# Kernel tuning notes

Measured on AMD Instinct MI355X. Metric: run time of the kernel, lower is better.

Reference implementation:

```python
import jax, jax.numpy as jnp
import numpy as np

DIM = 1024
HEADS = 16
DIM_HEAD = 64
INNER = HEADS * DIM_HEAD  # 1024
SCALE = DIM_HEAD ** -0.5


def setup_inputs() -> dict:
    key = jax.random.key(0)
    k1, k2, k3, k4 = jax.random.split(key, 4)
    B, N = 4, 2048
    x = jax.random.normal(k1, (B, N, DIM), dtype=jnp.float32)
    # Linear weights stored as [in, out] so y = x @ W (+ b)
    W_qkv = jax.random.normal(k2, (DIM, 3 * INNER), dtype=jnp.float32) * (DIM ** -0.5)
    W_out = jax.random.normal(k3, (INNER, DIM), dtype=jnp.float32) * (INNER ** -0.5)
    b_out = jax.random.normal(k4, (DIM,), dtype=jnp.float32) * 0.01
    return {"x": x, "W_qkv": W_qkv, "W_out": W_out, "b_out": b_out}


def reference(x, W_qkv, W_out, b_out):
    B, N, _ = x.shape
    qkv = x @ W_qkv  # [B, N, 3*INNER]
    q, k, v = jnp.split(qkv, 3, axis=-1)
    # [B, N, H, Dh] -> [B, H, N, Dh]
    reshape = lambda t: t.reshape(B, N, HEADS, DIM_HEAD).transpose(0, 2, 1, 3)
    q, k, v = reshape(q), reshape(k), reshape(v)
    dots = jnp.einsum("bhqd,bhkd->bhqk", q, k) * SCALE  # [B,H,N,N]
    attn = jax.nn.softmax(dots, axis=-1)
    out = jnp.einsum("bhqk,bhkd->bhqd", attn, v)  # [B,H,N,Dh]
    out = out.transpose(0, 2, 1, 3).reshape(B, N, INNER)
    return out @ W_out + b_out
```

## Files before the change

kernel.cpp:

```cpp
#include <hip/hip_runtime.h>


typedef _Float16 half8 __attribute__((ext_vector_type(8)));
typedef __fp16 fp16v2 __attribute__((ext_vector_type(2)));
typedef float floatx4 __attribute__((ext_vector_type(4)));
typedef unsigned short u16;

struct __align__(8) U16x4 { u16 x, y, z, w; };

__device__ __forceinline__ u16 f2h(float f) {
  union { _Float16 h; u16 u; } cv;
  cv.h = (_Float16)f;
  return cv.u;
}

__device__ __forceinline__ void g2l16(const void* g, void* l) {
  __builtin_amdgcn_global_load_lds(
      (const __attribute__((address_space(1))) void*)g,
      (__attribute__((address_space(3))) void*)l, 16, 0, 0);
}

__device__ __forceinline__ int swz(int c) { return (c & 3) ^ ((c >> 3) & 3); }
__device__ __forceinline__ int swz8(int s) { return (s & 7) ^ ((s >> 3) & 7); }

__global__ __launch_bounds__(256) void cast_f32_f16(const float* __restrict__ in,
                                                    u16* __restrict__ out) {
  long long base = ((long long)blockIdx.x * 256 + threadIdx.x) * 8;
  float4 a = *(const float4*)(in + base);
  float4 b = *(const float4*)(in + base + 4);
  U16x4 u0 = {f2h(a.x), f2h(a.y), f2h(a.z), f2h(a.w)};
  U16x4 u1 = {f2h(b.x), f2h(b.y), f2h(b.z), f2h(b.w)};
  *(U16x4*)(out + base) = u0;
  *(U16x4*)(out + base + 4) = u1;
}

__global__ __launch_bounds__(256) void transpose_cast(const float* __restrict__ in,
                                                      u16* __restrict__ out,
                                                      int K, int N) {
  __shared__ u16 ls[64][72];
  const int nTK = K >> 6;
  const int tk = blockIdx.x % nTK;
  const int tn = blockIdx.x / nTK;
  const int tid = threadIdx.x;
#pragma unroll
  for (int i = 0; i < 4; ++i) {
    int idx = i * 256 + tid;
    int r = idx >> 4, c4 = (idx & 15) * 4;
    float4 v = *(const float4*)(in + (long long)(tk * 64 + r) * N + tn * 64 + c4);
    ls[r][c4 + 0] = f2h(v.x);
    ls[r][c4 + 1] = f2h(v.y);
    ls[r][c4 + 2] = f2h(v.z);
    ls[r][c4 + 3] = f2h(v.w);
  }
  __syncthreads();
#pragma unroll
  for (int i = 0; i < 4; ++i) {
    int idx = i * 256 + tid;
    int nr = idx >> 4, kc4 = (idx & 15) * 4;
    U16x4 u = {ls[kc4 + 0][nr], ls[kc4 + 1][nr], ls[kc4 + 2][nr], ls[kc4 + 3][nr]};
    *(U16x4*)(out + (long long)(tn * 64 + nr) * K + tk * 64 + kc4) = u;
  }
}

template <int EPI>
__global__ __launch_bounds__(256, 4) void gemm_f16(const u16* __restrict__ A,
                                                   const u16* __restrict__ Bt,
                                                   u16* __restrict__ O0,
                                                   u16* __restrict__ O1,
                                                   u16* __restrict__ O2,
                                                   float* __restrict__ Of,
                                                   const float* __restrict__ bias) {
  __shared__ __attribute__((aligned(16))) u16 lsA[128 * 64];
  __shared__ __attribute__((aligned(16))) u16 lsB[128 * 64];
  const int tid = threadIdx.x;
  const int lane = tid & 63, wave = tid >> 6;
  const int l15 = lane & 15, quad = lane >> 4;
  const int w7 = l15 & 7;
  const int offk0 = ((quad) ^ w7) * 8;
  const int offk1 = ((4 + quad) ^ w7) * 8;
  const int wm = (wave >> 1) * 64, wn = (wave & 1) * 64;
  const int bm = blockIdx.x & 63;
  const int bn = blockIdx.x >> 6;

  const u16* ga[4];
  const u16* gb[4];
#pragma unroll
  for (int i = 0; i < 4; ++i) {
    int s = i * 256 + tid;
    ga[i] = A + (long long)(bm * 128 + (s >> 3)) * 1024 + swz8(s) * 8;
    gb[i] = Bt + (long long)(bn * 128 + (s >> 3)) * 1024 + swz8(s) * 8;
  }

  floatx4 acc[4][4] = {};

  for (int kt = 0; kt < 16; ++kt) {
    const int ko = kt * 64;
#pragma unroll
    for (int i = 0; i < 4; ++i)
      g2l16(ga[i] + ko, lsA + (i * 256 + wave * 64) * 8);
#pragma unroll
    for (int i = 0; i < 4; ++i)
      g2l16(gb[i] + ko, lsB + (i * 256 + wave * 64) * 8);
    __syncthreads();
#pragma unroll
    for (int ks = 0; ks < 2; ++ks) {
      const int off = ks ? offk1 : offk0;
      half8 af[4], bf[4];
#pragma unroll
      for (int mt = 0; mt < 4; ++mt)
        af[mt] = *(const half8*)(lsA + (wm + mt * 16 + l15) * 64 + off);
#pragma unroll
      for (int nt = 0; nt < 4; ++nt)
        bf[nt] = *(const half8*)(lsB + (wn + nt * 16 + l15) * 64 + off);
#pragma unroll
      for (int mt = 0; mt < 4; ++mt)
#pragma unroll
        for (int nt = 0; nt < 4; ++nt)
          acc[mt][nt] = __builtin_amdgcn_mfma_f32_16x16x32_f16(af[mt], bf[nt], acc[mt][nt], 0, 0, 0);
    }
    __syncthreads();
  }

  if (EPI == 0) {
    const float slq = 0.125f * 1.44269504088896f;
#pragma unroll
    for (int mt = 0; mt < 4; ++mt) {
      int gm = bm * 128 + wm + mt * 16 + quad * 4;
      int b = gm >> 11, n0 = gm & 2047;
#pragma unroll
      for (int nt = 0; nt < 4; ++nt) {
        int gc = bn * 128 + wn + nt * 16 + l15;
        int t = gc >> 10, hd = gc & 1023, h = hd >> 6, d = hd & 63;
        long long bh = (long long)(b * 16 + h);
        if (t == 2) {
          U16x4 u = {f2h(acc[mt][nt][0]), f2h(acc[mt][nt][1]),
                     f2h(acc[mt][nt][2]), f2h(acc[mt][nt][3])};
          *(U16x4*)(O2 + (bh * 64 + d) * 2048 + n0) = u;
        } else {
          float s = (t == 0) ? slq : 1.0f;
          u16* dst = (t == 0 ? O0 : O1) + (bh * 2048 + n0) * 64 + d;
#pragma unroll
          for (int r = 0; r < 4; ++r) dst[r * 64] = f2h(acc[mt][nt][r] * s);
        }
      }
    }
  } else {
#pragma unroll
    for (int mt = 0; mt < 4; ++mt) {
      int gm = bm * 128 + wm + mt * 16 + quad * 4;
#pragma unroll
      for (int nt = 0; nt < 4; ++nt) {
        int gc = bn * 128 + wn + nt * 16 + l15;
        float bv = bias[gc];
#pragma unroll
        for (int r = 0; r < 4; ++r)
          Of[(long long)(gm + r) * 1024 + gc] = acc[mt][nt][r] + bv;
      }
    }
  }
}

__global__ __launch_bounds__(256, 2) void attn_flash(const u16* __restrict__ Qh,
                                                     const u16* __restrict__ Kh,
                                                     const u16* __restrict__ Vt,
                                                     u16* __restrict__ Oh) {
  __shared__ __attribute__((aligned(16))) u16 lsK[2 * 2 * 64 * 32];
  __shared__ __attribute__((aligned(16))) u16 lsV[2 * 2 * 64 * 32];
  __shared__ __attribute__((aligned(16))) u16 lsP[4 * 64 * 32];
  const int tid = threadIdx.x;
  const int lane = tid & 63, wave = tid >> 6;
  const int l15 = lane & 15, quad = lane >> 4;
  const int sw = (l15 >> 1) & 3;
  const int qsw8 = (quad ^ sw) * 8;
  const int bh = blockIdx.x & 63, qt = blockIdx.x >> 6;
  const u16* Qb = Qh + ((long long)bh * 2048 + qt * 256) * 64;
  const u16* Kb = Kh + (long long)bh * 2048 * 64;
  const u16* Vb = Vt + (long long)bh * 64 * 2048;
  u16* lsPw = lsP + wave * 2048;

  half8 qb[4][2];
#pragma unroll
  for (int pass = 0; pass < 2; ++pass) {
#pragma unroll
    for (int i = 0; i < 4; ++i) {
      int c = i * 256 + tid;
      g2l16(Qb + (pass * 128 + ((c >> 2) & 127)) * 64 + (c >> 9) * 32 + swz(c) * 8,
            lsK + (i * 256 + wave * 64) * 8);
    }
    __syncthreads();
    if ((wave >> 1) == pass) {
      const int lrow = (wave & 1) * 64;
#pragma unroll
      for (int qt2 = 0; qt2 < 4; ++qt2)
#pragma unroll
        for (int ks = 0; ks < 2; ++ks)
          qb[qt2][ks] = *(const half8*)(lsK + ks * 4096 +
                                        (lrow + qt2 * 16 + l15) * 32 + qsw8);
    }
    __syncthreads();
  }

#pragma unroll
  for (int i = 0; i < 2; ++i) {
    int c = i * 256 + tid;
    g2l16(Kb + ((c >> 2) & 63) * 64 + (c >> 8) * 32 + swz(c) * 8,
          lsK + (i * 256 + wave * 64) * 8);
    g2l16(Vb + ((c >> 2) & 63) * 2048 + (c >> 8) * 32 + swz(c) * 8,
          lsV + (i * 256 + wave * 64) * 8);
  }

  half8 onesf;
#pragma unroll
  for (int j = 0; j < 8; ++j) onesf[j] = (_Float16)1.0f;

  floatx4 oacc[4][4] = {};
  floatx4 osum[4] = {};

  for (int kt = 0; kt < 32; ++kt) {
    const int cur = kt & 1;
    const u16* bufK = lsK + cur * 4096;
    const u16* bufV = lsV + cur * 4096;
    __syncthreads();
    if (kt < 31) {
      u16* nK = lsK + (1 - cur) * 4096;
      u16* nV = lsV + (1 - cur) * 4096;
#pragma unroll
      for (int i = 0; i < 2; ++i) {
        int c = i * 256 + tid;
        g2l16(Kb + (kt + 1) * 4096 + ((c >> 2) & 63) * 64 + (c >> 8) * 32 + swz(c) * 8,
              nK + (i * 256 + wave * 64) * 8);
        g2l16(Vb + ((c >> 2) & 63) * 2048 + (kt + 1) * 64 + (c >> 8) * 32 + swz(c) * 8,
              nV + (i * 256 + wave * 64) * 8);
      }
    }
#pragma unroll
    for (int ks4 = 0; ks4 < 2; ++ks4) {
      floatx4 sacc[2][4] = {};
      __builtin_amdgcn_s_setprio(1);
#pragma unroll
      for (int ks = 0; ks < 2; ++ks) {
#pragma unroll
        for (int h = 0; h < 2; ++h) {
          half8 kf = *(const half8*)(bufK + ks * 2048 + ((ks4 * 2 + h) * 16 + l15) * 32 + qsw8);
#pragma unroll
          for (int qt2 = 0; qt2 < 4; ++qt2)
            sacc[h][qt2] = __builtin_amdgcn_mfma_f32_16x16x32_f16(kf, qb[qt2][ks], sacc[h][qt2], 0, 0, 0);
        }
      }
      __builtin_amdgcn_s_setprio(0);
#pragma unroll
      for (int h = 0; h < 2; ++h) {
#pragma unroll
        for (int qt2 = 0; qt2 < 4; ++qt2) {
          float p0 = __builtin_amdgcn_exp2f(sacc[h][qt2][0]);
          float p1 = __builtin_amdgcn_exp2f(sacc[h][qt2][1]);
          float p2 = __builtin_amdgcn_exp2f(sacc[h][qt2][2]);
          float p3 = __builtin_amdgcn_exp2f(sacc[h][qt2][3]);
          union { fp16v2 h2; unsigned u; } lo, hi;
          lo.h2 = __builtin_amdgcn_cvt_pkrtz(p0, p1);
          hi.h2 = __builtin_amdgcn_cvt_pkrtz(p2, p3);
          uint2 pk = {lo.u, hi.u};
          *(uint2*)(lsPw + (qt2 * 16 + l15) * 32 +
                    (((2 * h + (quad >> 1)) ^ sw) * 8) + (quad & 1) * 4) = pk;
        }
      }
      half8 pa[4];
#pragma unroll
      for (int qt2 = 0; qt2 < 4; ++qt2)
        pa[qt2] = *(const half8*)(lsPw + (qt2 * 16 + l15) * 32 + qsw8);
      __builtin_amdgcn_s_setprio(1);
#pragma unroll
      for (int dt = 0; dt < 4; ++dt) {
        half8 vb = *(const half8*)(bufV + ks4 * 2048 + (dt * 16 + l15) * 32 + qsw8);
#pragma unroll
        for (int qt2 = 0; qt2 < 4; ++qt2)
          oacc[qt2][dt] = __builtin_amdgcn_mfma_f32_16x16x32_f16(pa[qt2], vb, oacc[qt2][dt], 0, 0, 0);
      }
#pragma unroll
      for (int qt2 = 0; qt2 < 4; ++qt2)
        osum[qt2] = __builtin_amdgcn_mfma_f32_16x16x32_f16(pa[qt2], onesf, osum[qt2], 0, 0, 0);
      __builtin_amdgcn_s_setprio(0);
    }
  }

  const int b = bh >> 4, h = bh & 15;
#pragma unroll
  for (int qt2 = 0; qt2 < 4; ++qt2) {
#pragma unroll
    for (int r = 0; r < 4; ++r) {
      float inv = 1.0f / osum[qt2][r];
      int qrow = qt * 256 + wave * 64 + qt2 * 16 + quad * 4 + r;
      long long rowbase = ((long long)b * 2048 + qrow) * 1024 + h * 64;
#pragma unroll
      for (int dt = 0; dt < 4; ++dt)
        Oh[rowbase + dt * 16 + l15] = f2h(oacc[qt2][dt][r] * inv);
    }
  }
}

extern "C" void kernel_launch(void* const* d_in, const int* in_sizes, int n_in,
                              void* d_out, int out_size, void* d_ws, size_t ws_size,
                              hipStream_t stream) {
  const float* x = (const float*)d_in[0];
  const float* Wqkv = (const float*)d_in[1];
  const float* Wout = (const float*)d_in[2];
  const float* bout = (const float*)d_in[3];
  float* out = (float*)d_out;

  char* ws = (char*)d_ws;
  u16* Xh = (u16*)(ws);
  u16* Wqkvt = (u16*)(ws + (16ll << 20));
  u16* Woutt = (u16*)(ws + (22ll << 20));
  u16* Qh = (u16*)(ws + (24ll << 20));
  u16* Kh = (u16*)(ws + (40ll << 20));
  u16* Vt = (u16*)(ws + (56ll << 20));
  u16* Oh = (u16*)(ws + (72ll << 20));

  cast_f32_f16<<<4096, 256, 0, stream>>>(x, Xh);
  transpose_cast<<<16 * 48, 256, 0, stream>>>(Wqkv, Wqkvt, 1024, 3072);
  transpose_cast<<<16 * 16, 256, 0, stream>>>(Wout, Woutt, 1024, 1024);
  gemm_f16<0><<<64 * 24, 256, 0, stream>>>(Xh, Wqkvt, Qh, Kh, Vt, nullptr, nullptr);
  attn_flash<<<512, 256, 0, stream>>>(Qh, Kh, Vt, Oh);
  gemm_f16<1><<<64 * 8, 256, 0, stream>>>(Oh, Woutt, nullptr, nullptr, nullptr, out, bout);
}
```

Before: 253.7 us.

## Split QKV GEMM into dedicated 256x256-tile kernel with triple-buffered async loads

Replaces the templated 128x128 GEMM used for the QKV projection with a dedicated 512-thread kernel computing 256x256 tiles. It uses a 3-stage ring of direct global-to-LDS loads with explicit vmcnt waits and a block-index remap meant to group tiles for L2 reuse. The output projection keeps the old kernel with only the bias epilogue. Larger tiles cut global and LDS traffic per FLOP, but the kernel runs one block per CU with higher register pressure, and 384 blocks may leave a ragged last wave across the CUs.

```diff
diff --git a/kernel.cpp b/kernel.cpp
--- a/kernel.cpp
+++ b/kernel.cpp
@@ -62,12 +62,114 @@
   }
 }
 
-template <int EPI>
-__global__ __launch_bounds__(256, 4) void gemm_f16(const u16* __restrict__ A,
+__global__ __launch_bounds__(512, 1) void qkv_gemm(const u16* __restrict__ A,
                                                    const u16* __restrict__ Bt,
                                                    u16* __restrict__ O0,
                                                    u16* __restrict__ O1,
-                                                   u16* __restrict__ O2,
+                                                   u16* __restrict__ O2) {
+  __shared__ __attribute__((aligned(16))) u16 lsA[3 * 8192];
+  __shared__ __attribute__((aligned(16))) u16 lsB[3 * 8192];
+  const int tid = threadIdx.x;
+  const int lane = tid & 63, wid = tid >> 6;
+  const int l15 = lane & 15, quad = lane >> 4;
+  const int rdoff = (quad ^ ((l15 >> 1) & 3)) * 8;
+  const int wr = (wid >> 2) * 128, wc = (wid & 3) * 64;
+  const int b = (blockIdx.x & 7) * 48 + (blockIdx.x >> 3);
+  const int bm = b & 31, bn = b >> 5;
+
+  const u16* gA[2];
+  const u16* gB[2];
+  int dst[2];
+#pragma unroll
+  for (int j = 0; j < 2; ++j) {
+    int sl = j * 512 + tid;
+    int r = sl >> 2, cc = sl & 3;
+    int csw = (cc ^ ((r >> 1) & 3)) * 8;
+    gA[j] = A + (long long)(bm * 256 + r) * 1024 + csw;
+    gB[j] = Bt + (long long)(bn * 256 + r) * 1024 + csw;
+    dst[j] = sl * 8;
+  }
+
+  floatx4 acc[8][4] = {};
+
+#pragma unroll
+  for (int t = 0; t < 2; ++t) {
+#pragma unroll
+    for (int j = 0; j < 2; ++j) g2l16(gA[j] + t * 32, lsA + t * 8192 + dst[j]);
+#pragma unroll
+    for (int j = 0; j < 2; ++j) g2l16(gB[j] + t * 32, lsB + t * 8192 + dst[j]);
+  }
+  asm volatile("s_waitcnt vmcnt(4)");
+  __builtin_amdgcn_s_barrier();
+
+  int cur = 0;
+  for (int t = 0; t < 32; ++t) {
+    const u16* bA = lsA + cur * 8192;
+    const u16* bB = lsB + cur * 8192;
+    half8 af[4], bf[4];
+#pragma unroll
+    for (int i = 0; i < 4; ++i)
+      bf[i] = *(const half8*)(bB + (wc + i * 16 + l15) * 32 + rdoff);
+#pragma unroll
+    for (int i = 0; i < 4; ++i)
+      af[i] = *(const half8*)(bA + (wr + i * 16 + l15) * 32 + rdoff);
+    if (t < 30) {
+      const int nb = cur ? cur - 1 : 2;
+      const int ko = (t + 2) * 32;
+#pragma unroll
+      for (int j = 0; j < 2; ++j) g2l16(gA[j] + ko, lsA + nb * 8192 + dst[j]);
+#pragma unroll
+      for (int j = 0; j < 2; ++j) g2l16(gB[j] + ko, lsB + nb * 8192 + dst[j]);
+    }
+    __builtin_amdgcn_s_barrier();
+#pragma unroll
+    for (int i = 0; i < 4; ++i)
+#pragma unroll
+      for (int nt = 0; nt < 4; ++nt)
+        acc[i][nt] = __builtin_amdgcn_mfma_f32_16x16x32_f16(af[i], bf[nt],
+                                                            acc[i][nt], 0, 0, 0);
+    half8 ag[4];
+#pragma unroll
+    for (int i = 0; i < 4; ++i)
+      ag[i] = *(const half8*)(bA + (wr + 64 + i * 16 + l15) * 32 + rdoff);
+#pragma unroll
+    for (int i = 0; i < 4; ++i)
+#pragma unroll
+      for (int nt = 0; nt < 4; ++nt)
+        acc[4 + i][nt] = __builtin_amdgcn_mfma_f32_16x16x32_f16(ag[i], bf[nt],
+                                                                acc[4 + i][nt], 0, 0, 0);
+    if (t < 30)       asm volatile("s_waitcnt vmcnt(4)");
+    else if (t == 30) asm volatile("s_waitcnt vmcnt(0)");
+    __builtin_amdgcn_s_barrier();
+    cur = cur == 2 ? 0 : cur + 1;
+  }
+
+  const float slq = 0.125f * 1.44269504088896f;
+#pragma unroll
+  for (int mt = 0; mt < 8; ++mt) {
+    int gm = bm * 256 + wr + (mt >> 2) * 64 + (mt & 3) * 16 + quad * 4;
+    int bb = gm >> 11, n0 = gm & 2047;
+#pragma unroll
+    for (int nt = 0; nt < 4; ++nt) {
+      int gc = bn * 256 + wc + nt * 16 + l15;
+      int tsel = gc >> 10, hd = gc & 1023, h = hd >> 6, d = hd & 63;
+      long long bh = (long long)(bb * 16 + h);
+      if (tsel == 2) {
+        U16x4 u = {f2h(acc[mt][nt][0]), f2h(acc[mt][nt][1]),
+                   f2h(acc[mt][nt][2]), f2h(acc[mt][nt][3])};
+        *(U16x4*)(O2 + (bh * 64 + d) * 2048 + n0) = u;
+      } else {
+        float s = (tsel == 0) ? slq : 1.0f;
+        u16* dstp = (tsel == 0 ? O0 : O1) + (bh * 2048 + n0) * 64 + d;
+#pragma unroll
+        for (int r = 0; r < 4; ++r) dstp[r * 64] = f2h(acc[mt][nt][r] * s);
+      }
+    }
+  }
+}
+
+__global__ __launch_bounds__(256, 4) void out_gemm(const u16* __restrict__ A,
+                                                   const u16* __restrict__ Bt,
                                                    float* __restrict__ Of,
                                                    const float* __restrict__ bias) {
   __shared__ __attribute__((aligned(16))) u16 lsA[128 * 64];
@@ -121,41 +223,16 @@
     __syncthreads();
   }
 
-  if (EPI == 0) {
-    const float slq = 0.125f * 1.44269504088896f;
-#pragma unroll
-    for (int mt = 0; mt < 4; ++mt) {
-      int gm = bm * 128 + wm + mt * 16 + quad * 4;
-      int b = gm >> 11, n0 = gm & 2047;
-#pragma unroll
-      for (int nt = 0; nt < 4; ++nt) {
-        int gc = bn * 128 + wn + nt * 16 + l15;
-        int t = gc >> 10, hd = gc & 1023, h = hd >> 6, d = hd & 63;
-        long long bh = (long long)(b * 16 + h);
-        if (t == 2) {
-          U16x4 u = {f2h(acc[mt][nt][0]), f2h(acc[mt][nt][1]),
-                     f2h(acc[mt][nt][2]), f2h(acc[mt][nt][3])};
-          *(U16x4*)(O2 + (bh * 64 + d) * 2048 + n0) = u;
-        } else {
-          float s = (t == 0) ? slq : 1.0f;
-          u16* dst = (t == 0 ? O0 : O1) + (bh * 2048 + n0) * 64 + d;
-#pragma unroll
-          for (int r = 0; r < 4; ++r) dst[r * 64] = f2h(acc[mt][nt][r] * s);
-        }
-      }
-    }
-  } else {
-#pragma unroll
-    for (int mt = 0; mt < 4; ++mt) {
-      int gm = bm * 128 + wm + mt * 16 + quad * 4;
-#pragma unroll
-      for (int nt = 0; nt < 4; ++nt) {
-        int gc = bn * 128 + wn + nt * 16 + l15;
-        float bv = bias[gc];
-#pragma unroll
-        for (int r = 0; r < 4; ++r)
-          Of[(long long)(gm + r) * 1024 + gc] = acc[mt][nt][r] + bv;
-      }
+#pragma unroll
+  for (int mt = 0; mt < 4; ++mt) {
+    int gm = bm * 128 + wm + mt * 16 + quad * 4;
+#pragma unroll
+    for (int nt = 0; nt < 4; ++nt) {
+      int gc = bn * 128 + wn + nt * 16 + l15;
+      float bv = bias[gc];
+#pragma unroll
+      for (int r = 0; r < 4; ++r)
+        Of[(long long)(gm + r) * 1024 + gc] = acc[mt][nt][r] + bv;
     }
   }
 }
@@ -319,7 +396,7 @@
   cast_f32_f16<<<4096, 256, 0, stream>>>(x, Xh);
   transpose_cast<<<16 * 48, 256, 0, stream>>>(Wqkv, Wqkvt, 1024, 3072);
   transpose_cast<<<16 * 16, 256, 0, stream>>>(Wout, Woutt, 1024, 1024);
-  gemm_f16<0><<<64 * 24, 256, 0, stream>>>(Xh, Wqkvt, Qh, Kh, Vt, nullptr, nullptr);
+  qkv_gemm<<<384, 512, 0, stream>>>(Xh, Wqkvt, Qh, Kh, Vt);
   attn_flash<<<512, 256, 0, stream>>>(Qh, Kh, Vt, Oh);
-  gemm_f16<1><<<64 * 8, 256, 0, stream>>>(Oh, Woutt, nullptr, nullptr, nullptr, out, bout);
-}
+  out_gemm<<<64 * 8, 256, 0, stream>>>(Oh, Woutt, out, bout);
+}
```

After: 270.3 us. +6.5%, slower.
